# Performance work log

Hardware: AMD Instinct MI355X
Metric: run time of the kernel (lower is better)

The kernel has to match this reference:

```python
import jax, jax.numpy as jnp
import numpy as np

WINDOW_SIZE = 11
SIGMA = 1.5
CHANNELS = 3
DATA_RANGE = 1.0


def _create_window(window_size, channel):
    x = np.arange(window_size) - window_size // 2
    g = np.exp(-(x ** 2) / (2.0 * SIGMA ** 2))
    g = g / g.sum()
    w2d = np.outer(g, g).astype(np.float32)  # [ws, ws]
    # depthwise kernel, OIHW with I=1, O=channel
    return jnp.asarray(np.broadcast_to(w2d, (channel, 1, window_size, window_size)).copy())


def _depthwise_conv(x, window, channel):
    # x: [B, C, H, W], window: [C, 1, ws, ws], VALID padding, groups=C
    return jax.lax.conv_general_dilated(
        x, window, window_strides=(1, 1), padding='VALID',
        dimension_numbers=('NCHW', 'OIHW', 'NCHW'),
        feature_group_count=channel)


def setup_inputs() -> dict:
    key = jax.random.key(0)
    k1, k2 = jax.random.split(key)
    img1 = jax.random.uniform(k1, (32, CHANNELS, 512, 512), dtype=jnp.float32)
    img2 = jax.random.uniform(k2, (32, CHANNELS, 512, 512), dtype=jnp.float32)
    return {"img1": img1, "img2": img2}


def reference(img1, img2):
    channel = img1.shape[1]
    window = _create_window(WINDOW_SIZE, channel).astype(img1.dtype)

    mu1 = _depthwise_conv(img1, window, channel)
    mu2 = _depthwise_conv(img2, window, channel)
    mu1_sq = mu1 * mu1
    mu2_sq = mu2 * mu2
    mu1_mu2 = mu1 * mu2

    sigma1_sq = _depthwise_conv(img1 * img1, window, channel) - mu1_sq
    sigma2_sq = _depthwise_conv(img2 * img2, window, channel) - mu2_sq
    sigma12 = _depthwise_conv(img1 * img2, window, channel) - mu1_mu2

    C1 = (0.01 * DATA_RANGE) ** 2
    C2 = (0.03 * DATA_RANGE) ** 2
    v1 = 2.0 * sigma12 + C2
    v2 = sigma1_sq + sigma2_sq + C2
    ssim_map = (2.0 * mu1_mu2 + C1) * v1 / ((mu1_sq + mu2_sq + C1) * v2)
    # mean over channel, height, width -> per-image SSIM [B]
    return ssim_map.mean(axis=(1, 2, 3))
```

## Files before the change

kernel.cpp:

```cpp
#include <hip/hip_runtime.h>
#include <math.h>

#define H 512
#define W 512
#define OUT_H 502
#define OUT_W 502
#define C1c 1.0e-4f
#define C2c 9.0e-4f

#define TH 56
#define NR (TH + 10)
#define NCOLS 256
#define HALO 10

__global__ __launch_bounds__(256, 4) void ssim_kernel(const float* __restrict__ img1,
                                                      const float* __restrict__ img2,
                                                      float* __restrict__ out) {
    __shared__ float2 ring[2][NCOLS + HALO];
    __shared__ float wsum[4];

    const int tid = threadIdx.x;

    float g[11];
    {
        float s = 0.f;
#pragma unroll
        for (int i = 0; i < 11; ++i) {
            float d = (float)(i - 5);
            g[i] = expf(-d * d * (1.0f / 4.5f));
            s += g[i];
        }
        float inv = 1.0f / s;
#pragma unroll
        for (int i = 0; i < 11; ++i) g[i] *= inv;
    }

    const int X0 = blockIdx.x * NCOLS;
    const int Y0 = blockIdx.y * TH;
    const int plane = blockIdx.z;
    const size_t pbase = (size_t)plane * (H * W);
    const float* __restrict__ p1 = img1 + pbase;
    const float* __restrict__ p2 = img2 + pbase;

    const int gx = X0 + tid;
    const int hx = min(X0 + NCOLS + tid, W - 1);

    float acc0[11], acc1[11], acc2[11], acc3[11], acc4[11];
#pragma unroll
    for (int i = 0; i < 11; ++i) { acc0[i]=0.f; acc1[i]=0.f; acc2[i]=0.f; acc3[i]=0.f; acc4[i]=0.f; }

    float lsum = 0.f;

    {
        const size_t rowoff = (size_t)min(Y0, H - 1) * W;
    }
    int gy0 = min(Y0, H - 1);
    float a1 = p1[(size_t)gy0 * W + gx];
    float a2 = p2[(size_t)gy0 * W + gx];
    float b1 = 0.f, b2 = 0.f;
    if (tid < HALO) { b1 = p1[(size_t)gy0 * W + hx]; b2 = p2[(size_t)gy0 * W + hx]; }

#pragma unroll 1
    for (int rb = 0; rb < NR; rb += 11) {
#pragma unroll
        for (int p = 0; p < 11; ++p) {
            const int r = rb + p;
            const int slot = r & 1;

            ring[slot][tid] = make_float2(a1, a2);
            if (tid < HALO) ring[slot][NCOLS + tid] = make_float2(b1, b2);

            {
                const int gy = min(Y0 + r + 1, H - 1);
                const size_t rowoff = (size_t)gy * W;
                a1 = p1[rowoff + gx];
                a2 = p2[rowoff + gx];
                if (tid < HALO) { b1 = p1[rowoff + hx]; b2 = p2[rowoff + hx]; }
            }

            __syncthreads();

            float h0 = 0.f, h1 = 0.f, h2 = 0.f, h3 = 0.f, h4 = 0.f;
            const float2* rp = &ring[slot][tid];
#pragma unroll
            for (int t = 0; t < 11; ++t) {
                const float2 v = rp[t];
                const float w = g[t];
                h0 = fmaf(w, v.x,       h0);
                h1 = fmaf(w, v.y,       h1);
                h2 = fmaf(w, v.x * v.x, h2);
                h3 = fmaf(w, v.y * v.y, h3);
                h4 = fmaf(w, v.x * v.y, h4);
            }

#pragma unroll
            for (int a = 0; a < 11; ++a) {
                const float w = g[(p - a + 11) % 11];
                acc0[a] = fmaf(w, h0, acc0[a]);
                acc1[a] = fmaf(w, h1, acc1[a]);
                acc2[a] = fmaf(w, h2, acc2[a]);
                acc3[a] = fmaf(w, h3, acc3[a]);
                acc4[a] = fmaf(w, h4, acc4[a]);
            }

            const int e = (p + 1) % 11;
            if (r >= 10) {
                const int oy = Y0 + r - 10;
                const float m1 = acc0[e], m2 = acc1[e];
                const float m1s = m1 * m1, m2s = m2 * m2, m12 = m1 * m2;
                const float sig1  = acc2[e] - m1s;
                const float sig2  = acc3[e] - m2s;
                const float sig12 = acc4[e] - m12;
                const float num = (2.f * m12 + C1c) * (2.f * sig12 + C2c);
                const float den = (m1s + m2s + C1c) * (sig1 + sig2 + C2c);
                const float v = num * __builtin_amdgcn_rcpf(den);
                if (gx < OUT_W && oy < OUT_H) lsum += v;
            }
            acc0[e] = 0.f; acc1[e] = 0.f; acc2[e] = 0.f; acc3[e] = 0.f; acc4[e] = 0.f;
        }
    }

#pragma unroll
    for (int off = 32; off > 0; off >>= 1) lsum += __shfl_down(lsum, off, 64);
    if ((tid & 63) == 0) wsum[tid >> 6] = lsum;
    __syncthreads();
    if (tid == 0) {
        const float inv_count = 1.0f / (3.0f * (float)OUT_H * (float)OUT_W);
        const float total = (wsum[0] + wsum[1] + wsum[2] + wsum[3]) * inv_count;
        atomicAdd(&out[plane / 3], total);
    }
}

__global__ void zero_out(float* out, int n) {
    int i = threadIdx.x + blockIdx.x * blockDim.x;
    if (i < n) out[i] = 0.f;
}

extern "C" void kernel_launch(void* const* d_in, const int* in_sizes, int n_in,
                              void* d_out, int out_size, void* d_ws, size_t ws_size,
                              hipStream_t stream) {
    const float* img1 = (const float*)d_in[0];
    const float* img2 = (const float*)d_in[1];
    float* out = (float*)d_out;

    zero_out<<<1, 64, 0, stream>>>(out, out_size);

    const int nplanes = in_sizes[0] / (H * W);
    dim3 grid(W / NCOLS,
              (OUT_H + TH - 1) / TH,
              nplanes);
    ssim_kernel<<<grid, 256, 0, stream>>>(img1, img2, out);
}
```

Baseline: 264.2 us.

## Process two columns per thread across full image width, removing halo loads

Each block now spans the whole 512-wide row with each thread handling two adjacent columns, loaded as float2 and stored to shared memory as float4. This removes the separate halo loads and the second column block, and it shares the shared-memory reads of the horizontal window between the two outputs. The last row tile is shifted up to stay in bounds and skips rows already covered by the previous tile. Gaussian weights are forced into scalar registers. Doubling the accumulator arrays raises register pressure, so occupancy is lowered to 2 blocks per SIMD, and the grid shrinks to half as many blocks.

```diff
diff --git a/kernel.cpp b/kernel.cpp
--- a/kernel.cpp
+++ b/kernel.cpp
@@ -10,13 +10,13 @@
 
 #define TH 56
 #define NR (TH + 10)
-#define NCOLS 256
-#define HALO 10
-
-__global__ __launch_bounds__(256, 4) void ssim_kernel(const float* __restrict__ img1,
-                                                      const float* __restrict__ img2,
-                                                      float* __restrict__ out) {
-    __shared__ float2 ring[2][NCOLS + HALO];
+#define RING_N 528
+
+__global__ __launch_bounds__(256, 2)
+void ssim_kernel(const float* __restrict__ img1,
+                 const float* __restrict__ img2,
+                 float* __restrict__ out) {
+    __shared__ float2 ring[2][RING_N];
     __shared__ float wsum[4];
 
     const int tid = threadIdx.x;
@@ -32,33 +32,42 @@
         }
         float inv = 1.0f / s;
 #pragma unroll
-        for (int i = 0; i < 11; ++i) g[i] *= inv;
-    }
-
-    const int X0 = blockIdx.x * NCOLS;
-    const int Y0 = blockIdx.y * TH;
-    const int plane = blockIdx.z;
+        for (int i = 0; i < 11; ++i) {
+            g[i] *= inv;
+            g[i] = __uint_as_float(__builtin_amdgcn_readfirstlane(__float_as_uint(g[i])));
+        }
+    }
+
+    const int oyb = blockIdx.x * TH;
+    const int Y0  = min(oyb, H - NR);
+    const int plane = blockIdx.y;
     const size_t pbase = (size_t)plane * (H * W);
     const float* __restrict__ p1 = img1 + pbase;
     const float* __restrict__ p2 = img2 + pbase;
 
-    const int gx = X0 + tid;
-    const int hx = min(X0 + NCOLS + tid, W - 1);
-
-    float acc0[11], acc1[11], acc2[11], acc3[11], acc4[11];
-#pragma unroll
-    for (int i = 0; i < 11; ++i) { acc0[i]=0.f; acc1[i]=0.f; acc2[i]=0.f; acc3[i]=0.f; acc4[i]=0.f; }
+    const int c0 = 2 * tid;
+    const bool v0ok = (c0 < OUT_W);
+    const bool v1ok = (c0 + 1 < OUT_W);
+
+    if (tid < RING_N - W) {
+        ring[0][W + tid] = make_float2(0.f, 0.f);
+        ring[1][W + tid] = make_float2(0.f, 0.f);
+    }
+
+    float a0A[11], a1A[11], a2A[11], a3A[11], a4A[11];
+    float a0B[11], a1B[11], a2B[11], a3B[11], a4B[11];
+#pragma unroll
+    for (int i = 0; i < 11; ++i) {
+        a0A[i]=0.f; a1A[i]=0.f; a2A[i]=0.f; a3A[i]=0.f; a4A[i]=0.f;
+        a0B[i]=0.f; a1B[i]=0.f; a2B[i]=0.f; a3B[i]=0.f; a4B[i]=0.f;
+    }
 
     float lsum = 0.f;
 
-    {
-        const size_t rowoff = (size_t)min(Y0, H - 1) * W;
-    }
-    int gy0 = min(Y0, H - 1);
-    float a1 = p1[(size_t)gy0 * W + gx];
-    float a2 = p2[(size_t)gy0 * W + gx];
-    float b1 = 0.f, b2 = 0.f;
-    if (tid < HALO) { b1 = p1[(size_t)gy0 * W + hx]; b2 = p2[(size_t)gy0 * W + hx]; }
+    int fidx = Y0 * W + c0;
+    const int fcap = (H - 1) * W + c0;
+    float2 va = *(const float2*)(p1 + fidx);
+    float2 vb = *(const float2*)(p2 + fidx);
 
 #pragma unroll 1
     for (int rb = 0; rb < NR; rb += 11) {
@@ -67,56 +76,97 @@
             const int r = rb + p;
             const int slot = r & 1;
 
-            ring[slot][tid] = make_float2(a1, a2);
-            if (tid < HALO) ring[slot][NCOLS + tid] = make_float2(b1, b2);
-
-            {
-                const int gy = min(Y0 + r + 1, H - 1);
-                const size_t rowoff = (size_t)gy * W;
-                a1 = p1[rowoff + gx];
-                a2 = p2[rowoff + gx];
-                if (tid < HALO) { b1 = p1[rowoff + hx]; b2 = p2[rowoff + hx]; }
-            }
+            *(float4*)&ring[slot][c0] = make_float4(va.x, vb.x, va.y, vb.y);
+
+            fidx = min(fidx + W, fcap);
+            va = *(const float2*)(p1 + fidx);
+            vb = *(const float2*)(p2 + fidx);
 
             __syncthreads();
 
-            float h0 = 0.f, h1 = 0.f, h2 = 0.f, h3 = 0.f, h4 = 0.f;
-            const float2* rp = &ring[slot][tid];
-#pragma unroll
-            for (int t = 0; t < 11; ++t) {
-                const float2 v = rp[t];
-                const float w = g[t];
-                h0 = fmaf(w, v.x,       h0);
-                h1 = fmaf(w, v.y,       h1);
-                h2 = fmaf(w, v.x * v.x, h2);
-                h3 = fmaf(w, v.y * v.y, h3);
-                h4 = fmaf(w, v.x * v.y, h4);
+            float hA0=0.f,hA1=0.f,hA2=0.f,hA3=0.f,hA4=0.f;
+            float hB0=0.f,hB1=0.f,hB2=0.f,hB3=0.f,hB4=0.f;
+            const float4* rp = (const float4*)&ring[slot][c0];
+#pragma unroll
+            for (int k = 0; k < 6; ++k) {
+                const float4 f = rp[k];
+                {
+                    const int e = 2 * k;
+                    const float x = f.x, y = f.y;
+                    const float q2 = x * x, q3 = y * y, q4 = x * y;
+                    if (e <= 10) {
+                        const float w = g[e];
+                        hA0 = fmaf(w, x,  hA0); hA1 = fmaf(w, y,  hA1);
+                        hA2 = fmaf(w, q2, hA2); hA3 = fmaf(w, q3, hA3);
+                        hA4 = fmaf(w, q4, hA4);
+                    }
+                    if (e >= 1) {
+                        const float w = g[e - 1];
+                        hB0 = fmaf(w, x,  hB0); hB1 = fmaf(w, y,  hB1);
+                        hB2 = fmaf(w, q2, hB2); hB3 = fmaf(w, q3, hB3);
+                        hB4 = fmaf(w, q4, hB4);
+                    }
+                }
+                {
+                    const int e = 2 * k + 1;
+                    const float x = f.z, y = f.w;
+                    const float q2 = x * x, q3 = y * y, q4 = x * y;
+                    if (e <= 10) {
+                        const float w = g[e];
+                        hA0 = fmaf(w, x,  hA0); hA1 = fmaf(w, y,  hA1);
+                        hA2 = fmaf(w, q2, hA2); hA3 = fmaf(w, q3, hA3);
+                        hA4 = fmaf(w, q4, hA4);
+                    }
+                    {
+                        const float w = g[e - 1];
+                        hB0 = fmaf(w, x,  hB0); hB1 = fmaf(w, y,  hB1);
+                        hB2 = fmaf(w, q2, hB2); hB3 = fmaf(w, q3, hB3);
+                        hB4 = fmaf(w, q4, hB4);
+                    }
+                }
             }
 
 #pragma unroll
             for (int a = 0; a < 11; ++a) {
                 const float w = g[(p - a + 11) % 11];
-                acc0[a] = fmaf(w, h0, acc0[a]);
-                acc1[a] = fmaf(w, h1, acc1[a]);
-                acc2[a] = fmaf(w, h2, acc2[a]);
-                acc3[a] = fmaf(w, h3, acc3[a]);
-                acc4[a] = fmaf(w, h4, acc4[a]);
+                a0A[a] = fmaf(w, hA0, a0A[a]); a1A[a] = fmaf(w, hA1, a1A[a]);
+                a2A[a] = fmaf(w, hA2, a2A[a]); a3A[a] = fmaf(w, hA3, a3A[a]);
+                a4A[a] = fmaf(w, hA4, a4A[a]);
+                a0B[a] = fmaf(w, hB0, a0B[a]); a1B[a] = fmaf(w, hB1, a1B[a]);
+                a2B[a] = fmaf(w, hB2, a2B[a]); a3B[a] = fmaf(w, hB3, a3B[a]);
+                a4B[a] = fmaf(w, hB4, a4B[a]);
             }
 
             const int e = (p + 1) % 11;
             if (r >= 10) {
                 const int oy = Y0 + r - 10;
-                const float m1 = acc0[e], m2 = acc1[e];
-                const float m1s = m1 * m1, m2s = m2 * m2, m12 = m1 * m2;
-                const float sig1  = acc2[e] - m1s;
-                const float sig2  = acc3[e] - m2s;
-                const float sig12 = acc4[e] - m12;
-                const float num = (2.f * m12 + C1c) * (2.f * sig12 + C2c);
-                const float den = (m1s + m2s + C1c) * (sig1 + sig2 + C2c);
-                const float v = num * __builtin_amdgcn_rcpf(den);
-                if (gx < OUT_W && oy < OUT_H) lsum += v;
+                if (oy >= oyb) {
+                    {
+                        const float m1 = a0A[e], m2 = a1A[e];
+                        const float m1s = m1 * m1, m2s = m2 * m2, m12 = m1 * m2;
+                        const float sig1  = a2A[e] - m1s;
+                        const float sig2  = a3A[e] - m2s;
+                        const float sig12 = a4A[e] - m12;
+                        const float num = (2.f * m12 + C1c) * (2.f * sig12 + C2c);
+                        const float den = (m1s + m2s + C1c) * (sig1 + sig2 + C2c);
+                        const float v = num * __builtin_amdgcn_rcpf(den);
+                        if (v0ok) lsum += v;
+                    }
+                    {
+                        const float m1 = a0B[e], m2 = a1B[e];
+                        const float m1s = m1 * m1, m2s = m2 * m2, m12 = m1 * m2;
+                        const float sig1  = a2B[e] - m1s;
+                        const float sig2  = a3B[e] - m2s;
+                        const float sig12 = a4B[e] - m12;
+                        const float num = (2.f * m12 + C1c) * (2.f * sig12 + C2c);
+                        const float den = (m1s + m2s + C1c) * (sig1 + sig2 + C2c);
+                        const float v = num * __builtin_amdgcn_rcpf(den);
+                        if (v1ok) lsum += v;
+                    }
+                }
             }
-            acc0[e] = 0.f; acc1[e] = 0.f; acc2[e] = 0.f; acc3[e] = 0.f; acc4[e] = 0.f;
+            a0A[e]=0.f; a1A[e]=0.f; a2A[e]=0.f; a3A[e]=0.f; a4A[e]=0.f;
+            a0B[e]=0.f; a1B[e]=0.f; a2B[e]=0.f; a3B[e]=0.f; a4B[e]=0.f;
         }
     }
 
@@ -146,8 +196,7 @@
     zero_out<<<1, 64, 0, stream>>>(out, out_size);
 
     const int nplanes = in_sizes[0] / (H * W);
-    dim3 grid(W / NCOLS,
-              (OUT_H + TH - 1) / TH,
+    dim3 grid((OUT_H + TH - 1) / TH,
               nplanes);
     ssim_kernel<<<grid, 256, 0, stream>>>(img1, img2, out);
 }
```

After: 261.5 us. Within noise of the previous version (-1.0%).

## Use full-row 512-thread blocks with taller strips and clamped overlap

Applied to the files above, without the earlier changes.

Each block now covers a whole 512-wide row with 512 threads, so the column halo loads and the thread-divergent halo branches go away. Strips are 67 output rows tall, and the last strip is clamped to start early; rows that overlap the previous strip are skipped in the sum. Row loads use a byte-offset pointer clamped to the last row and are issued after the barrier. Gaussian weights are made wave-uniform with readfirstlane, and the first tap initialises the accumulators instead of zeroing them. The bigger block and the higher occupancy target in the launch bounds may raise register pressure, and the grid drops to about 8 blocks per plane.

```diff
diff --git a/kernel.cpp b/kernel.cpp
--- a/kernel.cpp
+++ b/kernel.cpp
@@ -8,16 +8,16 @@
 #define C1c 1.0e-4f
 #define C2c 9.0e-4f
 
-#define TH 56
-#define NR (TH + 10)
-#define NCOLS 256
-#define HALO 10
+#define TH 67
+#define NR 77
+#define NT 512
 
-__global__ __launch_bounds__(256, 4) void ssim_kernel(const float* __restrict__ img1,
-                                                      const float* __restrict__ img2,
-                                                      float* __restrict__ out) {
-    __shared__ float2 ring[2][NCOLS + HALO];
-    __shared__ float wsum[4];
+__global__ __launch_bounds__(NT, 6)
+void ssim_kernel(const float* __restrict__ img1,
+                 const float* __restrict__ img2,
+                 float* __restrict__ out) {
+    __shared__ float2 ring[2][1024];
+    __shared__ float wsum[8];
 
     const int tid = threadIdx.x;
 
@@ -32,33 +32,36 @@
         }
         float inv = 1.0f / s;
 #pragma unroll
-        for (int i = 0; i < 11; ++i) g[i] *= inv;
+        for (int i = 0; i < 11; ++i) {
+            g[i] *= inv;
+            g[i] = __uint_as_float(__builtin_amdgcn_readfirstlane(__float_as_uint(g[i])));
+        }
     }
 
-    const int X0 = blockIdx.x * NCOLS;
-    const int Y0 = blockIdx.y * TH;
-    const int plane = blockIdx.z;
+    const int oyb = blockIdx.x * TH;
+    const int Y0  = min(oyb, H - NR);
+    const int plane = blockIdx.y;
     const size_t pbase = (size_t)plane * (H * W);
     const float* __restrict__ p1 = img1 + pbase;
     const float* __restrict__ p2 = img2 + pbase;
 
-    const int gx = X0 + tid;
-    const int hx = min(X0 + NCOLS + tid, W - 1);
+    const bool colok = (tid < OUT_W);
 
-    float acc0[11], acc1[11], acc2[11], acc3[11], acc4[11];
+    if (tid < 16) {
+        ring[0][W + tid] = make_float2(0.f, 0.f);
+        ring[1][W + tid] = make_float2(0.f, 0.f);
+    }
+
+    float a0[11], a1[11], a2[11], a3[11], a4[11];
 #pragma unroll
-    for (int i = 0; i < 11; ++i) { acc0[i]=0.f; acc1[i]=0.f; acc2[i]=0.f; acc3[i]=0.f; acc4[i]=0.f; }
+    for (int i = 0; i < 11; ++i) { a0[i]=0.f; a1[i]=0.f; a2[i]=0.f; a3[i]=0.f; a4[i]=0.f; }
 
     float lsum = 0.f;
 
-    {
-        const size_t rowoff = (size_t)min(Y0, H - 1) * W;
-    }
-    int gy0 = min(Y0, H - 1);
-    float a1 = p1[(size_t)gy0 * W + gx];
-    float a2 = p2[(size_t)gy0 * W + gx];
-    float b1 = 0.f, b2 = 0.f;
-    if (tid < HALO) { b1 = p1[(size_t)gy0 * W + hx]; b2 = p2[(size_t)gy0 * W + hx]; }
+    int foff = (Y0 * W + tid) * 4;
+    const int fcap = ((H - 1) * W + tid) * 4;
+    float va = *(const float*)((const char*)p1 + foff);
+    float vb = *(const float*)((const char*)p2 + foff);
 
 #pragma unroll 1
     for (int rb = 0; rb < NR; rb += 11) {
@@ -67,56 +70,60 @@
             const int r = rb + p;
             const int slot = r & 1;
 
-            ring[slot][tid] = make_float2(a1, a2);
-            if (tid < HALO) ring[slot][NCOLS + tid] = make_float2(b1, b2);
-
-            {
-                const int gy = min(Y0 + r + 1, H - 1);
-                const size_t rowoff = (size_t)gy * W;
-                a1 = p1[rowoff + gx];
-                a2 = p2[rowoff + gx];
-                if (tid < HALO) { b1 = p1[rowoff + hx]; b2 = p2[rowoff + hx]; }
-            }
+            ring[slot][tid] = make_float2(va, vb);
 
             __syncthreads();
 
-            float h0 = 0.f, h1 = 0.f, h2 = 0.f, h3 = 0.f, h4 = 0.f;
-            const float2* rp = &ring[slot][tid];
+            foff = min(foff + W * 4, fcap);
+            va = *(const float*)((const char*)p1 + foff);
+            vb = *(const float*)((const char*)p2 + foff);
+
+            float h0, h1, h2, h3, h4;
+            {
+                const float2* rp = &ring[slot][tid];
 #pragma unroll
-            for (int t = 0; t < 11; ++t) {
-                const float2 v = rp[t];
-                const float w = g[t];
-                h0 = fmaf(w, v.x,       h0);
-                h1 = fmaf(w, v.y,       h1);
-                h2 = fmaf(w, v.x * v.x, h2);
-                h3 = fmaf(w, v.y * v.y, h3);
-                h4 = fmaf(w, v.x * v.y, h4);
+                for (int t = 0; t < 11; ++t) {
+                    const float2 v = rp[t];
+                    const float w = g[t];
+                    const float q2 = v.x * v.x, q3 = v.y * v.y, q4 = v.x * v.y;
+                    if (t == 0) {
+                        h0 = w * v.x; h1 = w * v.y; h2 = w * q2; h3 = w * q3; h4 = w * q4;
+                    } else {
+                        h0 = fmaf(w, v.x, h0); h1 = fmaf(w, v.y, h1);
+                        h2 = fmaf(w, q2, h2);  h3 = fmaf(w, q3, h3);
+                        h4 = fmaf(w, q4, h4);
+                    }
+                }
             }
 
 #pragma unroll
             for (int a = 0; a < 11; ++a) {
                 const float w = g[(p - a + 11) % 11];
-                acc0[a] = fmaf(w, h0, acc0[a]);
-                acc1[a] = fmaf(w, h1, acc1[a]);
-                acc2[a] = fmaf(w, h2, acc2[a]);
-                acc3[a] = fmaf(w, h3, acc3[a]);
-                acc4[a] = fmaf(w, h4, acc4[a]);
+                if (a == p) {
+                    a0[a] = w * h0; a1[a] = w * h1; a2[a] = w * h2;
+                    a3[a] = w * h3; a4[a] = w * h4;
+                } else {
+                    a0[a] = fmaf(w, h0, a0[a]); a1[a] = fmaf(w, h1, a1[a]);
+                    a2[a] = fmaf(w, h2, a2[a]); a3[a] = fmaf(w, h3, a3[a]);
+                    a4[a] = fmaf(w, h4, a4[a]);
+                }
             }
 
-            const int e = (p + 1) % 11;
             if (r >= 10) {
+                const int e = (p + 1) % 11;
                 const int oy = Y0 + r - 10;
-                const float m1 = acc0[e], m2 = acc1[e];
-                const float m1s = m1 * m1, m2s = m2 * m2, m12 = m1 * m2;
-                const float sig1  = acc2[e] - m1s;
-                const float sig2  = acc3[e] - m2s;
-                const float sig12 = acc4[e] - m12;
-                const float num = (2.f * m12 + C1c) * (2.f * sig12 + C2c);
-                const float den = (m1s + m2s + C1c) * (sig1 + sig2 + C2c);
-                const float v = num * __builtin_amdgcn_rcpf(den);
-                if (gx < OUT_W && oy < OUT_H) lsum += v;
+                if (oy >= oyb) {
+                    const float m1 = a0[e], m2 = a1[e];
+                    const float m1s = m1 * m1, m2s = m2 * m2, m12 = m1 * m2;
+                    const float sig1  = a2[e] - m1s;
+                    const float sig2  = a3[e] - m2s;
+                    const float sig12 = a4[e] - m12;
+                    const float num = (2.f * m12 + C1c) * (2.f * sig12 + C2c);
+                    const float den = (m1s + m2s + C1c) * (sig1 + sig2 + C2c);
+                    const float v = num * __builtin_amdgcn_rcpf(den);
+                    if (colok) lsum += v;
+                }
             }
-            acc0[e] = 0.f; acc1[e] = 0.f; acc2[e] = 0.f; acc3[e] = 0.f; acc4[e] = 0.f;
         }
     }
 
@@ -126,8 +133,10 @@
     __syncthreads();
     if (tid == 0) {
         const float inv_count = 1.0f / (3.0f * (float)OUT_H * (float)OUT_W);
-        const float total = (wsum[0] + wsum[1] + wsum[2] + wsum[3]) * inv_count;
-        atomicAdd(&out[plane / 3], total);
+        float total = 0.f;
+#pragma unroll
+        for (int wv = 0; wv < 8; ++wv) total += wsum[wv];
+        atomicAdd(&out[plane / 3], total * inv_count);
     }
 }
 
@@ -146,8 +155,7 @@
     zero_out<<<1, 64, 0, stream>>>(out, out_size);
 
     const int nplanes = in_sizes[0] / (H * W);
-    dim3 grid(W / NCOLS,
-              (OUT_H + TH - 1) / TH,
+    dim3 grid((OUT_H + TH - 1) / TH,
               nplanes);
-    ssim_kernel<<<grid, 256, 0, stream>>>(img1, img2, out);
+    ssim_kernel<<<grid, NT, 0, stream>>>(img1, img2, out);
 }
```

Result: slower. 512.6 us (+94.0%).
